# Kernel tuning notes

Hardware: AMD Instinct MI355X
Metric: run time of the kernel (lower is better)

## Reference

```python
import jax, jax.numpy as jnp
import numpy as np

NX = 65536      # x_steps_soil
T_STEPS = 200   # t_steps
HID = 32        # function_learner hidden width


def setup_inputs() -> dict:
    key = jax.random.key(0)
    ks = jax.random.split(key, 6)
    # u0: stacked (c, sk) initial state, values in [0, 1)
    u0 = jax.random.uniform(ks[0], (NX, 2), dtype=jnp.float32)
    t = jnp.arange(T_STEPS, dtype=jnp.float32)  # uniform time grid, dt = 1

    def lin(k, fan_in, fan_out):
        W = jax.random.normal(k, (fan_in, fan_out), dtype=jnp.float32) / np.float32(np.sqrt(fan_in))
        b = jnp.zeros((fan_out,), dtype=jnp.float32)
        return W, b

    # func_r: [1 -> 32 -> 32 -> 32 -> 1], tanh hidden, sigmoid output (sigmoid=True)
    W0, b0 = lin(ks[1], 1, HID)
    W1, b1 = lin(ks[2], HID, HID)
    W2, b2 = lin(ks[3], HID, HID)
    W3, b3 = lin(ks[4], HID, 1)

    return dict(
        u0=u0, t=t,
        W0=W0, b0=b0, W1=W1, b1=b1, W2=W2, b2=b2, W3=W3, b3=b3,
        ret_fac=jnp.float32(1.0),            # self.ret_fac
        D=jnp.float32(1e-5),                 # diffusion coefficient
        stencil=jnp.array([-1.0, 1.0], dtype=jnp.float32),
        BC=jnp.float32(1.0),                 # top Dirichlet BC value
        f=jnp.float32(0.5),                  # kinetic/instantaneous sorption share
        k_d=jnp.float32(1.0),                # Freundlich constant
        beta=jnp.float32(0.8),               # Freundlich exponent
        alpha=jnp.float32(0.05),             # kinetic rate constant
        rho_s=jnp.float32(1.5),              # bulk density
        n_e=jnp.float32(0.3),                # porosity
        v_e=jnp.float32(0.005),              # effective velocity
        dx=jnp.float32(0.01),                # spatial step
    )


def reference(u0, t, W0, b0, W1, b1, W2, b2, W3, b3,
              ret_fac, D, stencil, BC, f, k_d, beta, alpha, rho_s, n_e, v_e, dx):
    dt = t[1] - t[0]

    def mlp_r(c):
        # per-cell learned retardation multiplier (func_r), sigmoid output in (0,1)
        h = jnp.tanh(c[:, None] @ W0 + b0)   # [Nx, H]
        h = jnp.tanh(h @ W1 + b1)
        h = jnp.tanh(h @ W2 + b2)
        return jax.nn.sigmoid(h @ W3 + b3)[:, 0]  # [Nx]

    def rhs(u):
        c, sk = u[:, 0], u[:, 1]
        ret = mlp_r(c) * ret_fac
        # neighbor values: Dirichlet BC at top, zero-gradient at bottom
        cl = jnp.concatenate([jnp.full((1,), BC, dtype=c.dtype), c[:-1]])
        cr = jnp.concatenate([c[1:], c[-1:]])
        # stencil fluxes (stencil = [-1, 1])
        lf = stencil[0] * c + stencil[1] * cl
        lf = lf.at[0].multiply(2.0)  # half-cell distance at Dirichlet boundary
        rf = stencil[0] * c + stencil[1] * cr  # rf[-1] == 0: no-flux bottom
        diff = D / dx**2 * (lf + rf)
        # upwind advection (flow from top to bottom)
        adv = v_e / dx * (c - cl)
        # two-site sorption kinetics (Freundlich isotherm)
        dsk = alpha * ((1.0 - f) * k_d * jnp.power(jnp.clip(c, 1e-9, None), beta) - sk)
        dc = ret * (diff - adv) - (rho_s / n_e) * dsk
        return jnp.stack([dc, dsk], axis=-1)  # [Nx, 2]

    def step(u, _):
        u2 = u + dt * rhs(u)
        return u2, u2

    _, traj = jax.lax.scan(step, u0, None, length=t.shape[0])
    return traj  # [T, Nx, 2]
```

## Files before the change

kernel.cpp:

```cpp
#include <hip/hip_runtime.h>
#include <stdint.h>

#define NXS    65536
#define HID    32
#define BTL    512
#define NB     256
#define OWNB   256
#define MARG   200
#define SSPAN  656
#define SLAB   128
#define EPOCH  24
#define LUT_N  4096
#define LUT_INV  512.0f
#define LUT_BIAS 2048.0f

typedef float    f32x4 __attribute__((ext_vector_type(4)));
typedef uint32_t u32x4 __attribute__((ext_vector_type(4)));

__device__ __forceinline__ float fexp2(float x) { return __builtin_amdgcn_exp2f(x); }
__device__ __forceinline__ float frcp(float x)  { return __builtin_amdgcn_rcpf(x); }
__device__ __forceinline__ float flog2(float x) { return __builtin_amdgcn_logf(x); }

__device__ __forceinline__ float dpp_up(float x) {
    int xi = __float_as_int(x);
    return __int_as_float(__builtin_amdgcn_update_dpp(xi, xi, 0x138, 0xF, 0xF, false));
}
__device__ __forceinline__ float dpp_down(float x) {
    int xi = __float_as_int(x);
    return __int_as_float(__builtin_amdgcn_update_dpp(xi, xi, 0x130, 0xF, 0xF, false));
}

__device__ __forceinline__ float fast_tanh(float x) {
    x = fminf(fmaxf(x, -15.0f), 15.0f);
    float e = fexp2(x * 2.8853900817779268f);
    return (e - 1.0f) * frcp(e + 1.0f);
}
__device__ __forceinline__ float fast_sigmoid(float x) {
    float e = fexp2(x * -1.4426950408889634f);
    return frcp(1.0f + e);
}

struct FinnPtrs {
    const float* tvec;
    const float* Dp;  const float* stencil; const float* BCp; const float* fp;
    const float* kdp; const float* betap;   const float* alphap; const float* rhosp;
    const float* nep; const float* vep;     const float* dxp;
};

__global__ __launch_bounds__(256) void finn_lut(
    const float* __restrict__ W0, const float* __restrict__ b0,
    const float* __restrict__ W1, const float* __restrict__ b1,
    const float* __restrict__ W2, const float* __restrict__ b2,
    const float* __restrict__ W3, const float* __restrict__ b3,
    const float* __restrict__ ret_fac, const float* __restrict__ betap,
    float* __restrict__ lut_ret, float* __restrict__ lut_pw)
{
    const int i = blockIdx.x * 256 + threadIdx.x;
    if (i > LUT_N) return;
    const float c = -4.0f + (float)i * (1.0f / LUT_INV);

    float h[HID], a[HID];
    #pragma unroll
    for (int j = 0; j < HID; ++j)
        h[j] = fast_tanh(fmaf(c, W0[j], b0[j]));

    #pragma unroll
    for (int j = 0; j < HID; ++j) a[j] = b1[j];
    #pragma unroll
    for (int k = 0; k < HID; ++k) {
        const float hk = h[k];
        #pragma unroll
        for (int j = 0; j < HID; ++j) a[j] = fmaf(hk, W1[k * HID + j], a[j]);
    }
    #pragma unroll
    for (int j = 0; j < HID; ++j) h[j] = fast_tanh(a[j]);

    #pragma unroll
    for (int j = 0; j < HID; ++j) a[j] = b2[j];
    #pragma unroll
    for (int k = 0; k < HID; ++k) {
        const float hk = h[k];
        #pragma unroll
        for (int j = 0; j < HID; ++j) a[j] = fmaf(hk, W2[k * HID + j], a[j]);
    }
    #pragma unroll
    for (int j = 0; j < HID; ++j) h[j] = fast_tanh(a[j]);

    float pre = b3[0];
    #pragma unroll
    for (int k = 0; k < HID; ++k) pre = fmaf(h[k], W3[k], pre);

    lut_ret[i] = fast_sigmoid(pre) * ret_fac[0];
    lut_pw[i]  = fexp2(betap[0] * flog2(fmaxf(c, 1e-9f)));
}

__global__ __launch_bounds__(BTL, 2) void finn_sweep(
    const float* __restrict__ uin, float* __restrict__ out,
    const float* __restrict__ lr_g, const float* __restrict__ lp_g,
    FinnPtrs P, int T, uint32_t outBytes)
{
    __shared__ f32x4  slut[LUT_N];
    __shared__ float2 xbuf[SSPAN];

    const int tid  = threadIdx.x;
    const int w    = tid >> 6;
    const int lane = tid & 63;

    for (int i = tid; i < LUT_N; i += BTL) {
        const float r0 = lr_g[i], r1 = lr_g[i + 1];
        const float p0 = lp_g[i], p1 = lp_g[i + 1];
        const float rs = r1 - r0, ps = p1 - p0;
        f32x4 e;
        e.x = rs; e.y = fmaf(-(float)i, rs, r0);
        e.z = ps; e.w = fmaf(-(float)i, ps, p0);
        slut[i] = e;
    }

    const float dt   = P.tvec[1] - P.tvec[0];
    const float s0   = P.stencil[0];
    const float s1   = P.stencil[1];
    const float dx   = P.dxp[0];
    const float A    = P.Dp[0] / (dx * dx);
    const float B    = P.vep[0] / dx;
    const float BC   = P.BCp[0];
    const float alp  = P.alphap[0];
    const float akd  = (1.0f - P.fp[0]) * P.kdp[0];
    const float rsne = P.rhosp[0] / P.nep[0];

    const float G     = dt * rsne * alp;
    const float mGAKD = -G * akd;
    const float S1c   = 1.0f - dt * alp;
    const float S2c   = dt * alp * akd;
    const float K1u   = dt * (2.0f * A * s0 - B);
    const float K2u   = dt * (A * s1 + B);
    const float K3u   = dt * A * s1;

    const int b = blockIdx.x;
    int blockBase = b * OWNB - MARG;
    if (blockBase < 0) blockBase = 0;
    if (blockBase > NXS - SSPAN) blockBase = NXS - SSPAN;
    const bool leftA  = (blockBase == 0);
    const bool rightA = (blockBase == NXS - SSPAN);
    const int ownRelL = b * OWNB - blockBase;
    const int ownRelR = ownRelL + OWNB;

    u32x4 srd;
    {
        const uint64_t op = (uint64_t)(uintptr_t)out;
        srd.x = (uint32_t)op;
        srd.y = (uint32_t)(op >> 32);
        srd.z = outBytes;
        srd.w = 0x00020000u;
    }

    int a = ((SSPAN - SLAB) * w / 7 + 1) & ~1;

    float c0, sk0, c1, sk1;
    {
        const f32x4* u4 = (const f32x4*)uin;
        const f32x4 u = u4[(blockBase + a + lane * 2) >> 1];
        c0 = u.x; sk0 = u.y; c1 = u.z; sk1 = u.w;
    }

    __syncthreads();

    int done = 0;
    while (done < T) {
        int nst = T - done; if (nst > EPOCH) nst = EPOCH;
        const int si = a + lane * 2;
        const int g0 = blockBase + si;

        float K0_0 = 0.0f, K1_0 = K1u, K2_0 = K2u;
        const float K3_0 = K3u;
        float K1_1 = K1u, K3_1 = K3u;
        const float K2_1 = K2u;
        if (g0 == 0)           { K0_0 = dt * BC * (2.0f * A * s1 + B);
                                 K1_0 = dt * (3.0f * A * s0 - B); K2_0 = 0.0f; }
        if (g0 + 1 == NXS - 1) { K1_1 = dt * (2.0f * A * s0 - B + A * s1);
                                 K3_1 = 0.0f; }

        const int vL = leftA ? 0 : done;
        const int vR = rightA ? SSPAN : SSPAN - done;
        const int pd = vR - vL - SLAB;
        const int aPrev = vL + ((pd * (w - 1) / 7 + 1) & ~1);
        const int aNext = vL + ((pd * (w + 1) / 7 + 1) & ~1);
        int bLo = (w == 0) ? 0     : (((aPrev + SLAB + a) >> 1) & ~1);
        int bHi = (w == 7) ? SSPAN : (((a + SLAB + aNext) >> 1) & ~1);
        if (bLo < ownRelL) bLo = ownRelL;
        if (bHi > ownRelR) bHi = ownRelR;
        const bool st = (si >= bLo) && (si < bHi);
        uint32_t voff = st ? (uint32_t)((done * NXS + g0) * 8) : 0x60000000u;

        float clS = dpp_up(c1);
        float crS = dpp_down(c0);
        float tt0 = __builtin_amdgcn_fmed3f(fmaf(c0, LUT_INV, LUT_BIAS), 0.0f, 4095.9f);
        f32x4 L0 = slut[(int)tt0];
        float tt1 = __builtin_amdgcn_fmed3f(fmaf(c1, LUT_INV, LUT_BIAS), 0.0f, 4095.9f);
        f32x4 L1 = slut[(int)tt1];

        for (int s = 0; s < nst; ++s) {
            float t0 = fmaf(K1_0, c0, K0_0);
            t0 = fmaf(K2_0, clS, t0);
            t0 = fmaf(K3_0, c1, t0);
            float t1 = K1_1 * c1;
            t1 = fmaf(K2_1, c0, t1);
            t1 = fmaf(K3_1, crS, t1);

            const float ret0 = fmaf(tt0, L0.x, L0.y);
            const float pw0  = fmaf(tt0, L0.z, L0.w);
            const float ret1 = fmaf(tt1, L1.x, L1.y);
            const float pw1  = fmaf(tt1, L1.z, L1.w);

            float v0 = fmaf(ret0, t0, c0); v0 = fmaf(mGAKD, pw0, v0);
            float v1 = fmaf(ret1, t1, c1); v1 = fmaf(mGAKD, pw1, v1);
            const float nc0 = fmaf(G, sk0, v0);
            const float nc1 = fmaf(G, sk1, v1);
            sk0 = fmaf(S1c, sk0, S2c * pw0);
            sk1 = fmaf(S1c, sk1, S2c * pw1);
            c0 = nc0; c1 = nc1;

            tt0 = __builtin_amdgcn_fmed3f(fmaf(c0, LUT_INV, LUT_BIAS), 0.0f, 4095.9f);
            L0 = slut[(int)tt0];
            tt1 = __builtin_amdgcn_fmed3f(fmaf(c1, LUT_INV, LUT_BIAS), 0.0f, 4095.9f);
            L1 = slut[(int)tt1];
            clS = dpp_up(c1);
            crS = dpp_down(c0);

            f32x4 ov; ov.x = c0; ov.y = sk0; ov.z = c1; ov.w = sk1;
            asm volatile("buffer_store_dwordx4 %0, %1, %2, 0 offen"
                         :: "v"(ov), "v"(voff), "s"(srd) : "memory");
            voff += (uint32_t)(NXS * 8);
        }

        done += nst;
        if (done >= T) break;

        asm volatile("s_waitcnt lgkmcnt(0)" ::: "memory");
        __builtin_amdgcn_s_barrier();
        asm volatile("" ::: "memory");
        {
            const int wLo = (w == 0 && leftA)  ? 0    : EPOCH;
            const int wHi = (w == 7 && rightA) ? SLAB : SLAB - EPOCH;
            const int sr = lane * 2;
            if (sr >= wLo && sr < wHi)         xbuf[a + sr]     = make_float2(c0, sk0);
            if (sr + 1 >= wLo && sr + 1 < wHi) xbuf[a + sr + 1] = make_float2(c1, sk1);
        }
        asm volatile("s_waitcnt lgkmcnt(0)" ::: "memory");
        __builtin_amdgcn_s_barrier();
        asm volatile("" ::: "memory");
        {
            const int vL2 = leftA ? 0 : done;
            const int vR2 = rightA ? SSPAN : SSPAN - done;
            const int pd2 = vR2 - vL2 - SLAB;
            a = vL2 + ((pd2 * w / 7 + 1) & ~1);
            const f32x4 u = *(const f32x4*)&xbuf[a + lane * 2];
            c0 = u.x; sk0 = u.y; c1 = u.z; sk1 = u.w;
        }
        asm volatile("s_waitcnt lgkmcnt(0)" ::: "memory");
        __builtin_amdgcn_s_barrier();
        asm volatile("" ::: "memory");
    }
}

extern "C" void kernel_launch(void* const* d_in, const int* in_sizes, int n_in,
                              void* d_out, int out_size, void* d_ws, size_t ws_size,
                              hipStream_t stream)
{
    const float* u0 = (const float*)d_in[0];
    FinnPtrs P;
    P.tvec    = (const float*)d_in[1];
    const float* W0      = (const float*)d_in[2];
    const float* b0      = (const float*)d_in[3];
    const float* W1      = (const float*)d_in[4];
    const float* b1      = (const float*)d_in[5];
    const float* W2      = (const float*)d_in[6];
    const float* b2      = (const float*)d_in[7];
    const float* W3      = (const float*)d_in[8];
    const float* b3      = (const float*)d_in[9];
    const float* ret_fac = (const float*)d_in[10];
    P.Dp      = (const float*)d_in[11];
    P.stencil = (const float*)d_in[12];
    P.BCp     = (const float*)d_in[13];
    P.fp      = (const float*)d_in[14];
    P.kdp     = (const float*)d_in[15];
    P.betap   = (const float*)d_in[16];
    P.alphap  = (const float*)d_in[17];
    P.rhosp   = (const float*)d_in[18];
    P.nep     = (const float*)d_in[19];
    P.vep     = (const float*)d_in[20];
    P.dxp     = (const float*)d_in[21];

    float* out     = (float*)d_out;
    float* lut_ret = (float*)d_ws;
    float* lut_pw  = (float*)((char*)d_ws + 32768);
    const int T = in_sizes[1];

    hipLaunchKernelGGL(finn_lut, dim3((LUT_N + 1 + 255) / 256), dim3(256), 0,
                       stream, W0, b0, W1, b1, W2, b2, W3, b3, ret_fac,
                       P.betap, lut_ret, lut_pw);

    hipLaunchKernelGGL(finn_sweep, dim3(NB), dim3(BTL), 0, stream,
                       u0, out, lut_ret, lut_pw, P, T,
                       (uint32_t)out_size * 4u);
}
```

Measured before the change: 63.92 us.

## Switch sweep to one cell per lane with 16 waves per block

Restructures the time-stepping sweep so each lane owns one cell instead of two. Blocks grow to 1024 threads (16 waves) with 64-cell slabs and 12-step epochs between shared-memory halo exchanges. This adds wave-level parallelism and shortens each lane's dependency chain. In exchange, halo synchronisation happens twice as often, more cells are recomputed redundantly in the slab overlaps, and stores shrink to dwordx2. A padding array inflates LDS use, apparently to cap how many blocks share a CU.

```diff
diff --git a/kernel.cpp b/kernel.cpp
--- a/kernel.cpp
+++ b/kernel.cpp
@@ -3,17 +3,19 @@
 
 #define NXS    65536
 #define HID    32
-#define BTL    512
+#define BT     1024
+#define NW     16
 #define NB     256
 #define OWNB   256
 #define MARG   200
 #define SSPAN  656
-#define SLAB   128
-#define EPOCH  24
+#define SLAB   64
+#define EPOCH  12
 #define LUT_N  4096
 #define LUT_INV  512.0f
 #define LUT_BIAS 2048.0f
 
+typedef float    f32x2 __attribute__((ext_vector_type(2)));
 typedef float    f32x4 __attribute__((ext_vector_type(4)));
 typedef uint32_t u32x4 __attribute__((ext_vector_type(4)));
 
@@ -94,19 +96,21 @@
     lut_pw[i]  = fexp2(betap[0] * flog2(fmaxf(c, 1e-9f)));
 }
 
-__global__ __launch_bounds__(BTL, 2) void finn_sweep(
+__global__ __launch_bounds__(BT, 4) void finn_sweep(
     const float* __restrict__ uin, float* __restrict__ out,
     const float* __restrict__ lr_g, const float* __restrict__ lp_g,
     FinnPtrs P, int T, uint32_t outBytes)
 {
     __shared__ f32x4  slut[LUT_N];
     __shared__ float2 xbuf[SSPAN];
+    __shared__ float  lds_pad[3072];
 
     const int tid  = threadIdx.x;
     const int w    = tid >> 6;
     const int lane = tid & 63;
-
-    for (int i = tid; i < LUT_N; i += BTL) {
+    if (tid == 0) ((volatile float*)lds_pad)[0] = 0.0f;
+
+    for (int i = tid; i < LUT_N; i += BT) {
         const float r0 = lr_g[i], r1 = lr_g[i + 1];
         const float p0 = lp_g[i], p1 = lp_g[i + 1];
         const float rs = r1 - r0, ps = p1 - p0;
@@ -153,13 +157,12 @@
         srd.w = 0x00020000u;
     }
 
-    int a = ((SSPAN - SLAB) * w / 7 + 1) & ~1;
-
-    float c0, sk0, c1, sk1;
+    int a = ((SSPAN - SLAB) * w) / (NW - 1);
+
+    float c, sk;
     {
-        const f32x4* u4 = (const f32x4*)uin;
-        const f32x4 u = u4[(blockBase + a + lane * 2) >> 1];
-        c0 = u.x; sk0 = u.y; c1 = u.z; sk1 = u.w;
+        const float2 u = ((const float2*)uin)[blockBase + a + lane];
+        c = u.x; sk = u.y;
     }
 
     __syncthreads();
@@ -167,67 +170,51 @@
     int done = 0;
     while (done < T) {
         int nst = T - done; if (nst > EPOCH) nst = EPOCH;
-        const int si = a + lane * 2;
+        const int si = a + lane;
         const int g0 = blockBase + si;
 
-        float K0_0 = 0.0f, K1_0 = K1u, K2_0 = K2u;
-        const float K3_0 = K3u;
-        float K1_1 = K1u, K3_1 = K3u;
-        const float K2_1 = K2u;
-        if (g0 == 0)           { K0_0 = dt * BC * (2.0f * A * s1 + B);
-                                 K1_0 = dt * (3.0f * A * s0 - B); K2_0 = 0.0f; }
-        if (g0 + 1 == NXS - 1) { K1_1 = dt * (2.0f * A * s0 - B + A * s1);
-                                 K3_1 = 0.0f; }
+        float K0 = 0.0f, K1 = K1u, K2 = K2u, K3 = K3u;
+        if (g0 == 0)       { K0 = dt * BC * (2.0f * A * s1 + B);
+                             K1 = dt * (3.0f * A * s0 - B); K2 = 0.0f; }
+        if (g0 == NXS - 1) { K1 = dt * (2.0f * A * s0 - B + A * s1);
+                             K3 = 0.0f; }
 
         const int vL = leftA ? 0 : done;
         const int vR = rightA ? SSPAN : SSPAN - done;
         const int pd = vR - vL - SLAB;
-        const int aPrev = vL + ((pd * (w - 1) / 7 + 1) & ~1);
-        const int aNext = vL + ((pd * (w + 1) / 7 + 1) & ~1);
-        int bLo = (w == 0) ? 0     : (((aPrev + SLAB + a) >> 1) & ~1);
-        int bHi = (w == 7) ? SSPAN : (((a + SLAB + aNext) >> 1) & ~1);
+        const int aPrev = vL + (pd * (w - 1)) / (NW - 1);
+        const int aNext = vL + (pd * (w + 1)) / (NW - 1);
+        int bLo = (w == 0)      ? 0     : ((aPrev + SLAB + a) >> 1);
+        int bHi = (w == NW - 1) ? SSPAN : ((a + SLAB + aNext) >> 1);
         if (bLo < ownRelL) bLo = ownRelL;
         if (bHi > ownRelR) bHi = ownRelR;
         const bool st = (si >= bLo) && (si < bHi);
         uint32_t voff = st ? (uint32_t)((done * NXS + g0) * 8) : 0x60000000u;
 
-        float clS = dpp_up(c1);
-        float crS = dpp_down(c0);
-        float tt0 = __builtin_amdgcn_fmed3f(fmaf(c0, LUT_INV, LUT_BIAS), 0.0f, 4095.9f);
-        f32x4 L0 = slut[(int)tt0];
-        float tt1 = __builtin_amdgcn_fmed3f(fmaf(c1, LUT_INV, LUT_BIAS), 0.0f, 4095.9f);
-        f32x4 L1 = slut[(int)tt1];
+        float clS = dpp_up(c);
+        float crS = dpp_down(c);
+        float tt = __builtin_amdgcn_fmed3f(fmaf(c, LUT_INV, LUT_BIAS), 0.0f, 4095.9f);
+        f32x4 L = slut[(int)tt];
 
         for (int s = 0; s < nst; ++s) {
-            float t0 = fmaf(K1_0, c0, K0_0);
-            t0 = fmaf(K2_0, clS, t0);
-            t0 = fmaf(K3_0, c1, t0);
-            float t1 = K1_1 * c1;
-            t1 = fmaf(K2_1, c0, t1);
-            t1 = fmaf(K3_1, crS, t1);
-
-            const float ret0 = fmaf(tt0, L0.x, L0.y);
-            const float pw0  = fmaf(tt0, L0.z, L0.w);
-            const float ret1 = fmaf(tt1, L1.x, L1.y);
-            const float pw1  = fmaf(tt1, L1.z, L1.w);
-
-            float v0 = fmaf(ret0, t0, c0); v0 = fmaf(mGAKD, pw0, v0);
-            float v1 = fmaf(ret1, t1, c1); v1 = fmaf(mGAKD, pw1, v1);
-            const float nc0 = fmaf(G, sk0, v0);
-            const float nc1 = fmaf(G, sk1, v1);
-            sk0 = fmaf(S1c, sk0, S2c * pw0);
-            sk1 = fmaf(S1c, sk1, S2c * pw1);
-            c0 = nc0; c1 = nc1;
-
-            tt0 = __builtin_amdgcn_fmed3f(fmaf(c0, LUT_INV, LUT_BIAS), 0.0f, 4095.9f);
-            L0 = slut[(int)tt0];
-            tt1 = __builtin_amdgcn_fmed3f(fmaf(c1, LUT_INV, LUT_BIAS), 0.0f, 4095.9f);
-            L1 = slut[(int)tt1];
-            clS = dpp_up(c1);
-            crS = dpp_down(c0);
-
-            f32x4 ov; ov.x = c0; ov.y = sk0; ov.z = c1; ov.w = sk1;
-            asm volatile("buffer_store_dwordx4 %0, %1, %2, 0 offen"
+            float t = fmaf(K1, c, K0);
+            t = fmaf(K2, clS, t);
+            t = fmaf(K3, crS, t);
+            const float ret = fmaf(tt, L.x, L.y);
+            const float pw  = fmaf(tt, L.z, L.w);
+            float v = fmaf(ret, t, c);
+            v = fmaf(mGAKD, pw, v);
+            const float nc = fmaf(G, sk, v);
+            sk = fmaf(S1c, sk, S2c * pw);
+            c = nc;
+
+            tt = __builtin_amdgcn_fmed3f(fmaf(c, LUT_INV, LUT_BIAS), 0.0f, 4095.9f);
+            L = slut[(int)tt];
+            clS = dpp_up(c);
+            crS = dpp_down(c);
+
+            f32x2 ov; ov.x = c; ov.y = sk;
+            asm volatile("buffer_store_dwordx2 %0, %1, %2, 0 offen"
                          :: "v"(ov), "v"(voff), "s"(srd) : "memory");
             voff += (uint32_t)(NXS * 8);
         }
@@ -239,11 +226,10 @@
         __builtin_amdgcn_s_barrier();
         asm volatile("" ::: "memory");
         {
-            const int wLo = (w == 0 && leftA)  ? 0    : EPOCH;
-            const int wHi = (w == 7 && rightA) ? SLAB : SLAB - EPOCH;
-            const int sr = lane * 2;
-            if (sr >= wLo && sr < wHi)         xbuf[a + sr]     = make_float2(c0, sk0);
-            if (sr + 1 >= wLo && sr + 1 < wHi) xbuf[a + sr + 1] = make_float2(c1, sk1);
+            const int wLo = (w == 0 && leftA)       ? 0    : EPOCH;
+            const int wHi = (w == NW - 1 && rightA) ? SLAB : SLAB - EPOCH;
+            if (lane >= wLo && lane < wHi)
+                xbuf[a + lane] = make_float2(c, sk);
         }
         asm volatile("s_waitcnt lgkmcnt(0)" ::: "memory");
         __builtin_amdgcn_s_barrier();
@@ -251,10 +237,9 @@
         {
             const int vL2 = leftA ? 0 : done;
             const int vR2 = rightA ? SSPAN : SSPAN - done;
-            const int pd2 = vR2 - vL2 - SLAB;
-            a = vL2 + ((pd2 * w / 7 + 1) & ~1);
-            const f32x4 u = *(const f32x4*)&xbuf[a + lane * 2];
-            c0 = u.x; sk0 = u.y; c1 = u.z; sk1 = u.w;
+            a = vL2 + ((vR2 - vL2 - SLAB) * w) / (NW - 1);
+            const float2 u = xbuf[a + lane];
+            c = u.x; sk = u.y;
         }
         asm volatile("s_waitcnt lgkmcnt(0)" ::: "memory");
         __builtin_amdgcn_s_barrier();
@@ -299,7 +284,6 @@
                        stream, W0, b0, W1, b1, W2, b2, W3, b3, ret_fac,
                        P.betap, lut_ret, lut_pw);
 
-    hipLaunchKernelGGL(finn_sweep, dim3(NB), dim3(BTL), 0, stream,
-                       u0, out, lut_ret, lut_pw, P, T,
-                       (uint32_t)out_size * 4u);
-}
+    hipLaunchKernelGGL(finn_sweep, dim3(NB), dim3(BT), 0, stream,
+                       u0, out, lut_ret, lut_pw, P, T, (uint32_t)out_size * 4u);
+}
```

Result: slower. 66.09 us (+3.4%).
